# Kernel optimization log

Hardware: AMD Instinct MI355X
Metric: run time of the kernel (lower is better)

## Reference

```python
import jax, jax.numpy as jnp
import numpy as np

ITER_ROUTING = 3


def squash(t):
    # t: [..., H]
    norm = jnp.sum(t * t, axis=-1)                      # [...]
    scale = norm / (1.0 + norm)
    return scale[..., None] * t / jnp.sqrt(norm)[..., None]


def setup_inputs() -> dict:
    key = jax.random.key(0)
    k1, k2 = jax.random.split(key)
    C, K, H = 1024, 64, 512  # H = 2 * hidden_size, hidden_size = 256
    encoder_output = jax.random.normal(k1, (C, K, H), dtype=jnp.float32)
    # nn.Linear(H, H, bias=False): weight W has shape [H_out, H_in], y = x @ W.T
    W = jax.random.normal(k2, (H, H), dtype=jnp.float32) * (1.0 / np.sqrt(H))
    return {"encoder_output": encoder_output, "W": W}


def reference(encoder_output, W):
    C, K, H = encoder_output.shape
    # Linear projection is identical every iteration in the original loop;
    # compute once (same math, same values).
    x_hat = jnp.einsum('ckh,gh->ckg', encoder_output, W)  # [C, K, H]
    b = jnp.zeros((C, K), dtype=encoder_output.dtype)
    c = None
    for _ in range(ITER_ROUTING):
        d = jax.nn.softmax(b, axis=-1)                    # [C, K]
        c_hat = jnp.sum(x_hat * d[..., None], axis=1)     # [C, H]
        c = squash(c_hat)                                 # [C, H]
        b = b + jnp.einsum('ckh,ch->ck', x_hat, c)        # agreement update
    return c
```

## Files before the change

### kernel.cpp

```cpp
#include <hip/hip_runtime.h>
#include <math.h>


#define KC 64
#define HD 512
#define NT 512

typedef _Float16 half8  __attribute__((ext_vector_type(8)));
typedef _Float16 half4v __attribute__((ext_vector_type(4)));
typedef float    f32x4  __attribute__((ext_vector_type(4)));

__launch_bounds__(256)
__global__ void cast_w_kernel(const float* __restrict__ W, _Float16* __restrict__ Wp) {
    int u    = blockIdx.x * 256 + threadIdx.x;
    int lane = u & 63;
    int j    = (u >> 6) & 3;
    int ks   = (u >> 8) & 1;
    int hs   = (u >> 9) & 7;
    int wv   = (u >> 12) & 7;
    int g  = wv * 64 + j * 16 + (lane & 15);
    int h0 = hs * 64 + ks * 32 + (lane >> 4) * 8;
    const float4* src = reinterpret_cast<const float4*>(W + (size_t)g * HD + h0);
    float4 a = src[0], b = src[1];
    half8 h = { (_Float16)a.x, (_Float16)a.y, (_Float16)a.z, (_Float16)a.w,
                (_Float16)b.x, (_Float16)b.y, (_Float16)b.z, (_Float16)b.w };
    *reinterpret_cast<half8*>(Wp + (size_t)u * 8) = h;
}

__launch_bounds__(NT, 2)
__global__ void proj_kernel(const float* __restrict__ enc,
                            const _Float16* __restrict__ Wp,
                            _Float16* __restrict__ xhat) {
    __shared__ _Float16 slab[8][8][64][8];

    const int tid  = threadIdx.x;
    const int lane = tid & 63;
    const int wave = tid >> 6;
    const int l15  = lane & 15, l4 = lane >> 4;
    const int c    = blockIdx.x;
    const float* ebase = enc + (size_t)c * (KC * HD);
    const _Float16* wbase = Wp + ((size_t)wave << 15) + (lane << 3);

    const int r0   = tid >> 4;
    const int c40  = (tid & 15) << 2;
    const int ks_w = c40 >> 5;
    const int l4g  = (c40 >> 3) & 3;
    const int e0w  = c40 & 7;
    const int prow = (l4g * 16 + (r0 & 15)) ^ (l4g << 1);
    const int p0   = (r0 >> 4) * 2 + ks_w;
    const int p1   = p0 + 4;
    const int plane_r = lane ^ ((lane >> 4) << 1);

    half8 bf[2][8];
    auto bload = [&](int hs) {
        #pragma unroll
        for (int q = 0; q < 8; ++q)
            bf[hs & 1][q] = *reinterpret_cast<const half8*>(wbase + hs * 4096 + q * 512);
    };

    float4 ev[8][2];
    #pragma unroll
    for (int hs = 0; hs < 8; ++hs) {
        ev[hs][0] = *reinterpret_cast<const float4*>(ebase + (size_t)r0 * HD + hs * 64 + c40);
        ev[hs][1] = *reinterpret_cast<const float4*>(ebase + (size_t)(r0 + 32) * HD + hs * 64 + c40);
    }
    bload(0);
    #pragma unroll
    for (int hs = 0; hs < 8; ++hs) {
        float4 v0 = ev[hs][0], v1 = ev[hs][1];
        half4v h0 = { (_Float16)v0.x, (_Float16)v0.y, (_Float16)v0.z, (_Float16)v0.w };
        half4v h1 = { (_Float16)v1.x, (_Float16)v1.y, (_Float16)v1.z, (_Float16)v1.w };
        *reinterpret_cast<half4v*>(&slab[hs][p0][prow][e0w]) = h0;
        *reinterpret_cast<half4v*>(&slab[hs][p1][prow][e0w]) = h1;
    }

    f32x4 acc[16];
    #pragma unroll
    for (int i = 0; i < 16; ++i) acc[i] = (f32x4){0.f, 0.f, 0.f, 0.f};

    __syncthreads();

    #pragma unroll
    for (int hs = 0; hs < 8; ++hs) {
        if (hs < 7) bload(hs + 1);
        #pragma unroll
        for (int ks = 0; ks < 2; ++ks) {
            half8 af[4];
            #pragma unroll
            for (int i = 0; i < 4; ++i)
                af[i] = *reinterpret_cast<const half8*>(&slab[hs][i * 2 + ks][plane_r][0]);
            #pragma unroll
            for (int i = 0; i < 4; ++i)
                #pragma unroll
                for (int j = 0; j < 4; ++j)
                    acc[i * 4 + j] = __builtin_amdgcn_mfma_f32_16x16x32_f16(
                        af[i], bf[hs & 1][ks * 4 + j], acc[i * 4 + j], 0, 0, 0);
        }
    }

    _Float16* xrow = xhat + (size_t)c * (KC * HD);
    #pragma unroll
    for (int i = 0; i < 4; ++i) {
        #pragma unroll
        for (int j = 0; j < 4; ++j) {
            f32x4 v = acc[i * 4 + j];
            const int g  = wave * 64 + j * 16 + l15;
            const int kb = i * 16 + l4 * 4;
            #pragma unroll
            for (int r = 0; r < 4; ++r)
                xrow[(size_t)(kb + r) * HD + g] = (_Float16)v[r];
        }
    }
}

__launch_bounds__(NT, 2)
__global__ void route_kernel(const _Float16* __restrict__ xhat,
                             float* __restrict__ out) {
    __shared__ _Float16 xh[KC][520];
    __shared__ float chatL[HD];
    __shared__ float dL[KC];
    __shared__ float bdotL[KC];
    __shared__ float red[8];

    const int tid  = threadIdx.x;
    const int lane = tid & 63;
    const int wave = tid >> 6;
    const int c    = blockIdx.x;
    const _Float16* xsrc = xhat + (size_t)c * (KC * HD);

    #pragma unroll
    for (int q = 0; q < 8; ++q) {
        int flat = tid + q * 512;
        int row  = flat >> 6;
        int col  = (flat & 63) << 3;
        half8 v = *reinterpret_cast<const half8*>(xsrc + (size_t)row * HD + col);
        *reinterpret_cast<half8*>(&xh[row][col]) = v;
    }
    __syncthreads();

    float breg = 0.0f;
    float alpha = 0.0f;

    #pragma unroll
    for (int it = 0; it < 3; ++it) {
        if (it > 0) {
            breg += bdotL[lane];
            float m = breg;
            #pragma unroll
            for (int off = 32; off; off >>= 1) m = fmaxf(m, __shfl_xor(m, off));
            float e = expf(breg - m);
            float se = e;
            #pragma unroll
            for (int off = 32; off; off >>= 1) se += __shfl_xor(se, off);
            if (wave == 0) dL[lane] = e / se;
            __syncthreads();
        }

        {
            float cs = 0.f;
            if (it == 0) {
                #pragma unroll 8
                for (int k = 0; k < KC; ++k) cs += (float)xh[k][tid];
                cs *= (1.0f / 64.0f);
            } else {
                #pragma unroll 8
                for (int k = 0; k < KC; ++k) cs += dL[k] * (float)xh[k][tid];
            }
            chatL[tid] = cs;
            float p = cs * cs;
            #pragma unroll
            for (int off = 32; off; off >>= 1) p += __shfl_xor(p, off);
            if (lane == 0) red[wave] = p;
        }
        __syncthreads();
        {
            float n2 = red[0] + red[1] + red[2] + red[3]
                     + red[4] + red[5] + red[6] + red[7];
            alpha = sqrtf(n2) / (1.0f + n2);
        }

        if (it < 2) {
            float4 cA = *reinterpret_cast<const float4*>(&chatL[lane * 8]);
            float4 cB = *reinterpret_cast<const float4*>(&chatL[lane * 8 + 4]);
            #pragma unroll
            for (int kk = 0; kk < 8; ++kk) {
                int k = wave * 8 + kk;
                half8 x = *reinterpret_cast<const half8*>(&xh[k][lane * 8]);
                float p = (float)x[0] * cA.x + (float)x[1] * cA.y
                        + (float)x[2] * cA.z + (float)x[3] * cA.w
                        + (float)x[4] * cB.x + (float)x[5] * cB.y
                        + (float)x[6] * cB.z + (float)x[7] * cB.w;
                #pragma unroll
                for (int off = 32; off; off >>= 1) p += __shfl_xor(p, off);
                if (lane == 0) bdotL[k] = alpha * p;
            }
            __syncthreads();
        } else {
            out[(size_t)c * HD + tid] = alpha * chatL[tid];
        }
    }
}

__launch_bounds__(NT, 2)
__global__ void fused_kernel(const float* __restrict__ enc,
                             const _Float16* __restrict__ Wp,
                             float* __restrict__ out) {
    __shared__ _Float16 slab[8][8][64][8];
    __shared__ float chatL[HD];
    __shared__ float bpart[2][8][KC];
    __shared__ float redp[2][8];

    const int tid  = threadIdx.x;
    const int lane = tid & 63;
    const int wave = tid >> 6;
    const int l15  = lane & 15, l4 = lane >> 4;
    const int c    = blockIdx.x;
    const float* ebase = enc + (size_t)c * (KC * HD);
    const _Float16* wbase = Wp + ((size_t)wave << 15) + (lane << 3);

    const int r0   = tid >> 4;
    const int c40  = (tid & 15) << 2;
    const int ks_w = c40 >> 5;
    const int l4g  = (c40 >> 3) & 3;
    const int e0w  = c40 & 7;
    const int prow = (l4g * 16 + (r0 & 15)) ^ (l4g << 1);
    const int p0   = (r0 >> 4) * 2 + ks_w;
    const int p1   = p0 + 4;
    const int plane_r = lane ^ ((lane >> 4) << 1);

    half8 bf[2][8];
    auto bload = [&](int hs) {
        #pragma unroll
        for (int q = 0; q < 8; ++q)
            bf[hs & 1][q] = *reinterpret_cast<const half8*>(wbase + hs * 4096 + q * 512);
    };

    float4 ev[8][2];
    #pragma unroll
    for (int hs = 0; hs < 8; ++hs) {
        ev[hs][0] = *reinterpret_cast<const float4*>(ebase + (size_t)r0 * HD + hs * 64 + c40);
        ev[hs][1] = *reinterpret_cast<const float4*>(ebase + (size_t)(r0 + 32) * HD + hs * 64 + c40);
    }
    bload(0);
    #pragma unroll
    for (int hs = 0; hs < 8; ++hs) {
        float4 v0 = ev[hs][0], v1 = ev[hs][1];
        half4v h0 = { (_Float16)v0.x, (_Float16)v0.y, (_Float16)v0.z, (_Float16)v0.w };
        half4v h1 = { (_Float16)v1.x, (_Float16)v1.y, (_Float16)v1.z, (_Float16)v1.w };
        *reinterpret_cast<half4v*>(&slab[hs][p0][prow][e0w]) = h0;
        *reinterpret_cast<half4v*>(&slab[hs][p1][prow][e0w]) = h1;
    }

    f32x4 acc[16];
    #pragma unroll
    for (int i = 0; i < 16; ++i) acc[i] = (f32x4){0.f, 0.f, 0.f, 0.f};

    __syncthreads();

    #pragma unroll
    for (int hs = 0; hs < 8; ++hs) {
        if (hs < 7) bload(hs + 1);
        #pragma unroll
        for (int ks = 0; ks < 2; ++ks) {
            half8 af[4];
            #pragma unroll
            for (int i = 0; i < 4; ++i)
                af[i] = *reinterpret_cast<const half8*>(&slab[hs][i * 2 + ks][plane_r][0]);
            #pragma unroll
            for (int i = 0; i < 4; ++i)
                #pragma unroll
                for (int j = 0; j < 4; ++j)
                    acc[i * 4 + j] = __builtin_amdgcn_mfma_f32_16x16x32_f16(
                        af[i], bf[hs & 1][ks * 4 + j], acc[i * 4 + j], 0, 0, 0);
        }
    }

    float breg = 0.0f;
    float chv[4];
    {
        #pragma unroll
        for (int j = 0; j < 4; ++j) chv[j] = 0.f;
        #pragma unroll
        for (int i = 0; i < 4; ++i)
            #pragma unroll
            for (int r = 0; r < 4; ++r) {
                #pragma unroll
                for (int j = 0; j < 4; ++j)
                    chv[j] += (1.0f / 64.0f) * acc[i * 4 + j][r];
            }
        #pragma unroll
        for (int j = 0; j < 4; ++j) {
            chv[j] += __shfl_xor(chv[j], 16);
            chv[j] += __shfl_xor(chv[j], 32);
        }
        float p = chv[0] * chv[0] + chv[1] * chv[1] + chv[2] * chv[2] + chv[3] * chv[3];
        #pragma unroll
        for (int off = 1; off <= 8; off <<= 1) p += __shfl_xor(p, off);
        if (lane == 0) redp[0][wave] = p;
        #pragma unroll
        for (int i = 0; i < 4; ++i)
            #pragma unroll
            for (int r = 0; r < 4; ++r) {
                float s = acc[i * 4 + 0][r] * chv[0] + acc[i * 4 + 1][r] * chv[1]
                        + acc[i * 4 + 2][r] * chv[2] + acc[i * 4 + 3][r] * chv[3];
                #pragma unroll
                for (int off = 1; off <= 8; off <<= 1) s += __shfl_xor(s, off);
                if (l15 == 0) bpart[0][wave][i * 16 + l4 * 4 + r] = s;
            }
        __syncthreads();
    }
    #pragma unroll
    for (int it = 1; it < 3; ++it) {
        const int rp = (it - 1) & 1, wp = it & 1;
        float n2 = 0.f;
        #pragma unroll
        for (int w = 0; w < 8; ++w) n2 += redp[rp][w];
        float alpha = sqrtf(n2) / (1.0f + n2);
        float dot = 0.f;
        #pragma unroll
        for (int w = 0; w < 8; ++w) dot += bpart[rp][w][lane];
        breg += alpha * dot;
        float m = breg;
        #pragma unroll
        for (int off = 32; off; off >>= 1) m = fmaxf(m, __shfl_xor(m, off));
        float e = expf(breg - m);
        float se = e;
        #pragma unroll
        for (int off = 32; off; off >>= 1) se += __shfl_xor(se, off);
        float dl = e / se;
        #pragma unroll
        for (int j = 0; j < 4; ++j) chv[j] = 0.f;
        #pragma unroll
        for (int i = 0; i < 4; ++i)
            #pragma unroll
            for (int r = 0; r < 4; ++r) {
                float dk = __shfl(dl, i * 16 + l4 * 4 + r);
                #pragma unroll
                for (int j = 0; j < 4; ++j)
                    chv[j] += dk * acc[i * 4 + j][r];
            }
        #pragma unroll
        for (int j = 0; j < 4; ++j) {
            chv[j] += __shfl_xor(chv[j], 16);
            chv[j] += __shfl_xor(chv[j], 32);
        }
        float p = chv[0] * chv[0] + chv[1] * chv[1] + chv[2] * chv[2] + chv[3] * chv[3];
        #pragma unroll
        for (int off = 1; off <= 8; off <<= 1) p += __shfl_xor(p, off);
        if (lane == 0) redp[wp][wave] = p;

        if (it < 2) {
            #pragma unroll
            for (int i = 0; i < 4; ++i)
                #pragma unroll
                for (int r = 0; r < 4; ++r) {
                    float s = acc[i * 4 + 0][r] * chv[0] + acc[i * 4 + 1][r] * chv[1]
                            + acc[i * 4 + 2][r] * chv[2] + acc[i * 4 + 3][r] * chv[3];
                    #pragma unroll
                    for (int off = 1; off <= 8; off <<= 1) s += __shfl_xor(s, off);
                    if (l15 == 0) bpart[wp][wave][i * 16 + l4 * 4 + r] = s;
                }
            __syncthreads();
        } else {
            if (l4 == 0) {
                #pragma unroll
                for (int j = 0; j < 4; ++j)
                    chatL[wave * 64 + j * 16 + l15] = chv[j];
            }
            __syncthreads();
            float n2f = 0.f;
            #pragma unroll
            for (int w = 0; w < 8; ++w) n2f += redp[wp][w];
            float alphaf = sqrtf(n2f) / (1.0f + n2f);
            out[(size_t)c * HD + tid] = alphaf * chatL[tid];
        }
    }
}

extern "C" void kernel_launch(void* const* d_in, const int* in_sizes, int n_in,
                              void* d_out, int out_size, void* d_ws, size_t ws_size,
                              hipStream_t stream) {
    const float* enc = (const float*)d_in[0];
    const float* W   = (const float*)d_in[1];
    float* out       = (float*)d_out;
    _Float16* Wp     = (_Float16*)d_ws;
    (void)in_sizes; (void)n_in; (void)out_size;

    const size_t wp_bytes   = (size_t)512 * 1024;
    const size_t xhat_bytes = (size_t)1024 * KC * HD * sizeof(_Float16);

    cast_w_kernel<<<128, 256, 0, stream>>>(W, Wp);
    if (ws_size >= wp_bytes + xhat_bytes) {
        _Float16* xhat = (_Float16*)((char*)d_ws + wp_bytes);
        proj_kernel<<<1024, NT, 0, stream>>>(enc, Wp, xhat);
        route_kernel<<<1024, NT, 0, stream>>>(xhat, out);
    } else {
        fused_kernel<<<1024, NT, 0, stream>>>(enc, Wp, out);
    }
}
```

Before: 100.1 us.

## Split projection blocks over K halves and stage output through LDS for coalesced stores

The projection kernel now launches two blocks per capsule, each handling 32 of the 64 K rows. This halves the LDS slab and accumulator registers and raises the occupancy hint to 4 blocks per CU. Results are staged in shared memory and written out as coalesced 16-byte rows instead of scattered 2-byte stores. In exchange, the W fragments are reloaded by twice as many blocks and the W prefetch double-buffering is dropped, which can expose load latency.

Measured after the change: 102.0 us. Within noise of the previous version (+1.9%).

```diff
diff --git a/kernel.cpp b/kernel.cpp
--- a/kernel.cpp
+++ b/kernel.cpp
@@ -4,7 +4,6 @@
 
 #define KC 64
 #define HD 512
-#define NT 512
 
 typedef _Float16 half8  __attribute__((ext_vector_type(8)));
 typedef _Float16 half4v __attribute__((ext_vector_type(4)));
@@ -27,18 +26,19 @@
     *reinterpret_cast<half8*>(Wp + (size_t)u * 8) = h;
 }
 
-__launch_bounds__(NT, 2)
+__launch_bounds__(512, 4)
 __global__ void proj_kernel(const float* __restrict__ enc,
                             const _Float16* __restrict__ Wp,
                             _Float16* __restrict__ xhat) {
-    __shared__ _Float16 slab[8][8][64][8];
+    __shared__ _Float16 slab[8][4][64][8];
 
     const int tid  = threadIdx.x;
     const int lane = tid & 63;
     const int wave = tid >> 6;
     const int l15  = lane & 15, l4 = lane >> 4;
-    const int c    = blockIdx.x;
-    const float* ebase = enc + (size_t)c * (KC * HD);
+    const int c    = blockIdx.x >> 1;
+    const int kh   = blockIdx.x & 1;
+    const float* ebase = enc + ((size_t)c * KC + kh * 32) * HD;
     const _Float16* wbase = Wp + ((size_t)wave << 15) + (lane << 3);
 
     const int r0   = tid >> 4;
@@ -48,72 +48,92 @@
     const int e0w  = c40 & 7;
     const int prow = (l4g * 16 + (r0 & 15)) ^ (l4g << 1);
     const int p0   = (r0 >> 4) * 2 + ks_w;
-    const int p1   = p0 + 4;
     const int plane_r = lane ^ ((lane >> 4) << 1);
 
-    half8 bf[2][8];
-    auto bload = [&](int hs) {
+    {
+        float4 e0 = *reinterpret_cast<const float4*>(ebase + (size_t)r0 * HD + 0 * 64 + c40);
+        float4 e1 = *reinterpret_cast<const float4*>(ebase + (size_t)r0 * HD + 1 * 64 + c40);
+        float4 e2 = *reinterpret_cast<const float4*>(ebase + (size_t)r0 * HD + 2 * 64 + c40);
+        float4 e3 = *reinterpret_cast<const float4*>(ebase + (size_t)r0 * HD + 3 * 64 + c40);
+        half4v h0 = { (_Float16)e0.x, (_Float16)e0.y, (_Float16)e0.z, (_Float16)e0.w };
+        half4v h1 = { (_Float16)e1.x, (_Float16)e1.y, (_Float16)e1.z, (_Float16)e1.w };
+        half4v h2 = { (_Float16)e2.x, (_Float16)e2.y, (_Float16)e2.z, (_Float16)e2.w };
+        half4v h3 = { (_Float16)e3.x, (_Float16)e3.y, (_Float16)e3.z, (_Float16)e3.w };
+        *reinterpret_cast<half4v*>(&slab[0][p0][prow][e0w]) = h0;
+        *reinterpret_cast<half4v*>(&slab[1][p0][prow][e0w]) = h1;
+        *reinterpret_cast<half4v*>(&slab[2][p0][prow][e0w]) = h2;
+        *reinterpret_cast<half4v*>(&slab[3][p0][prow][e0w]) = h3;
+    }
+    {
+        float4 e0 = *reinterpret_cast<const float4*>(ebase + (size_t)r0 * HD + 4 * 64 + c40);
+        float4 e1 = *reinterpret_cast<const float4*>(ebase + (size_t)r0 * HD + 5 * 64 + c40);
+        float4 e2 = *reinterpret_cast<const float4*>(ebase + (size_t)r0 * HD + 6 * 64 + c40);
+        float4 e3 = *reinterpret_cast<const float4*>(ebase + (size_t)r0 * HD + 7 * 64 + c40);
+        half4v h0 = { (_Float16)e0.x, (_Float16)e0.y, (_Float16)e0.z, (_Float16)e0.w };
+        half4v h1 = { (_Float16)e1.x, (_Float16)e1.y, (_Float16)e1.z, (_Float16)e1.w };
+        half4v h2 = { (_Float16)e2.x, (_Float16)e2.y, (_Float16)e2.z, (_Float16)e2.w };
+        half4v h3 = { (_Float16)e3.x, (_Float16)e3.y, (_Float16)e3.z, (_Float16)e3.w };
+        *reinterpret_cast<half4v*>(&slab[4][p0][prow][e0w]) = h0;
+        *reinterpret_cast<half4v*>(&slab[5][p0][prow][e0w]) = h1;
+        *reinterpret_cast<half4v*>(&slab[6][p0][prow][e0w]) = h2;
+        *reinterpret_cast<half4v*>(&slab[7][p0][prow][e0w]) = h3;
+    }
+
+    f32x4 acc[8];
+    #pragma unroll
+    for (int i = 0; i < 8; ++i) acc[i] = (f32x4){0.f, 0.f, 0.f, 0.f};
+
+    __syncthreads();
+
+    half8 bf[8];
+    #pragma unroll
+    for (int hs = 0; hs < 8; ++hs) {
         #pragma unroll
         for (int q = 0; q < 8; ++q)
-            bf[hs & 1][q] = *reinterpret_cast<const half8*>(wbase + hs * 4096 + q * 512);
-    };
-
-    float4 ev[8][2];
-    #pragma unroll
-    for (int hs = 0; hs < 8; ++hs) {
-        ev[hs][0] = *reinterpret_cast<const float4*>(ebase + (size_t)r0 * HD + hs * 64 + c40);
-        ev[hs][1] = *reinterpret_cast<const float4*>(ebase + (size_t)(r0 + 32) * HD + hs * 64 + c40);
-    }
-    bload(0);
-    #pragma unroll
-    for (int hs = 0; hs < 8; ++hs) {
-        float4 v0 = ev[hs][0], v1 = ev[hs][1];
-        half4v h0 = { (_Float16)v0.x, (_Float16)v0.y, (_Float16)v0.z, (_Float16)v0.w };
-        half4v h1 = { (_Float16)v1.x, (_Float16)v1.y, (_Float16)v1.z, (_Float16)v1.w };
-        *reinterpret_cast<half4v*>(&slab[hs][p0][prow][e0w]) = h0;
-        *reinterpret_cast<half4v*>(&slab[hs][p1][prow][e0w]) = h1;
-    }
-
-    f32x4 acc[16];
-    #pragma unroll
-    for (int i = 0; i < 16; ++i) acc[i] = (f32x4){0.f, 0.f, 0.f, 0.f};
-
-    __syncthreads();
-
-    #pragma unroll
-    for (int hs = 0; hs < 8; ++hs) {
-        if (hs < 7) bload(hs + 1);
+            bf[q] = *reinterpret_cast<const half8*>(wbase + hs * 4096 + q * 512);
         #pragma unroll
         for (int ks = 0; ks < 2; ++ks) {
-            half8 af[4];
-            #pragma unroll
-            for (int i = 0; i < 4; ++i)
+            half8 af[2];
+            #pragma unroll
+            for (int i = 0; i < 2; ++i)
                 af[i] = *reinterpret_cast<const half8*>(&slab[hs][i * 2 + ks][plane_r][0]);
             #pragma unroll
-            for (int i = 0; i < 4; ++i)
+            for (int i = 0; i < 2; ++i)
                 #pragma unroll
                 for (int j = 0; j < 4; ++j)
                     acc[i * 4 + j] = __builtin_amdgcn_mfma_f32_16x16x32_f16(
-                        af[i], bf[hs & 1][ks * 4 + j], acc[i * 4 + j], 0, 0, 0);
-        }
-    }
-
-    _Float16* xrow = xhat + (size_t)c * (KC * HD);
-    #pragma unroll
-    for (int i = 0; i < 4; ++i) {
+                        af[i], bf[ks * 4 + j], acc[i * 4 + j], 0, 0, 0);
+        }
+    }
+
+    __syncthreads();
+    _Float16 (*xo)[HD] = reinterpret_cast<_Float16 (*)[HD]>(&slab[0][0][0][0]);
+    #pragma unroll
+    for (int i = 0; i < 2; ++i) {
         #pragma unroll
         for (int j = 0; j < 4; ++j) {
             f32x4 v = acc[i * 4 + j];
             const int g  = wave * 64 + j * 16 + l15;
             const int kb = i * 16 + l4 * 4;
             #pragma unroll
-            for (int r = 0; r < 4; ++r)
-                xrow[(size_t)(kb + r) * HD + g] = (_Float16)v[r];
+            for (int r = 0; r < 4; ++r) xo[kb + r][g] = (_Float16)v[r];
+        }
+    }
+    __syncthreads();
+    {
+        _Float16* xrow = xhat + ((size_t)c * KC + kh * 32) * HD;
+        #pragma unroll
+        for (int q = 0; q < 4; ++q) {
+            int flat = tid + q * 512;
+            int row  = flat >> 6;
+            int col  = (flat & 63) << 3;
+            half8 v = *reinterpret_cast<const half8*>(&xo[row][col]);
+            *reinterpret_cast<half8*>(xrow + (size_t)row * HD + col) = v;
         }
     }
 }
 
-__launch_bounds__(NT, 2)
+__launch_bounds__(512, 2)
 __global__ void route_kernel(const _Float16* __restrict__ xhat,
                              float* __restrict__ out) {
     __shared__ _Float16 xh[KC][520];
@@ -201,7 +221,7 @@
     }
 }
 
-__launch_bounds__(NT, 2)
+__launch_bounds__(512, 2)
 __global__ void fused_kernel(const float* __restrict__ enc,
                              const _Float16* __restrict__ Wp,
                              float* __restrict__ out) {
@@ -392,9 +412,9 @@
     cast_w_kernel<<<128, 256, 0, stream>>>(W, Wp);
     if (ws_size >= wp_bytes + xhat_bytes) {
         _Float16* xhat = (_Float16*)((char*)d_ws + wp_bytes);
-        proj_kernel<<<1024, NT, 0, stream>>>(enc, Wp, xhat);
-        route_kernel<<<1024, NT, 0, stream>>>(xhat, out);
+        proj_kernel<<<2048, 512, 0, stream>>>(enc, Wp, xhat);
+        route_kernel<<<1024, 512, 0, stream>>>(xhat, out);
     } else {
-        fused_kernel<<<1024, NT, 0, stream>>>(enc, Wp, out);
+        fused_kernel<<<1024, 512, 0, stream>>>(enc, Wp, out);
     }
 }
```
